# Kernel optimization log

Measured on AMD Instinct MI355X. Metric: run time of the kernel, lower is better.

## Reference

```python
import jax, jax.numpy as jnp
import numpy as np

DIM = 512
HEADS = 8
DIM_HEAD = 64
INNER = HEADS * DIM_HEAD
SCALE = DIM_HEAD ** -0.5


def setup_inputs() -> dict:
    key = jax.random.key(0)
    ks = jax.random.split(key, 7)
    B, N = 8, 1024
    x = jax.random.normal(ks[0], (B, N, DIM), dtype=jnp.float32)
    rel_pos_bias = jax.random.normal(ks[1], (HEADS, N, N), dtype=jnp.float32) * 0.02
    w_qkv = jax.random.normal(ks[2], (DIM, 3 * INNER), dtype=jnp.float32) * (DIM ** -0.5)
    w_out = jax.random.normal(ks[3], (INNER, DIM), dtype=jnp.float32) * (INNER ** -0.5)
    b_out = jnp.zeros((DIM,), dtype=jnp.float32)
    ln_gamma = jnp.ones((DIM,), dtype=jnp.float32)
    ln_beta = jnp.zeros((DIM,), dtype=jnp.float32)
    return {"x": x, "rel_pos_bias": rel_pos_bias, "w_qkv": w_qkv,
            "w_out": w_out, "b_out": b_out, "ln_gamma": ln_gamma, "ln_beta": ln_beta}


def _layernorm(x, gamma, beta, eps=1e-5):
    mu = jnp.mean(x, axis=-1, keepdims=True)
    var = jnp.var(x, axis=-1, keepdims=True)
    return (x - mu) * jax.lax.rsqrt(var + eps) * gamma + beta


def reference(x, rel_pos_bias, w_qkv, w_out, b_out, ln_gamma, ln_beta):
    B, N, _ = x.shape
    xn = _layernorm(x, ln_gamma, ln_beta)
    qkv = xn @ w_qkv  # [B,N,3*INNER]
    q, k, v = jnp.split(qkv, 3, axis=-1)
    # b n (h d) -> b h n d
    reshape = lambda t: t.reshape(B, N, HEADS, DIM_HEAD).transpose(0, 2, 1, 3)
    q, k, v = reshape(q) * SCALE, reshape(k), reshape(v)
    sim = jnp.einsum('bhid,bhjd->bhij', q, k)
    sim = sim + rel_pos_bias  # broadcast [h,N,N] over batch
    attn = jax.nn.softmax(sim, axis=-1)
    out = jnp.einsum('bhij,bhjd->bhid', attn, v)
    out = out.transpose(0, 2, 1, 3).reshape(B, N, INNER)
    return out @ w_out + b_out
```

## Files before the change

### kernel.cpp

```cpp
#include <hip/hip_runtime.h>
#include <hip/hip_bf16.h>

#define DIM 512
#define HEADS 8
#define DHEAD 64
#define INNER 512
#define NSEQ 1024
#define BATCH 8
#define MROWS (BATCH*NSEQ)
#define QK_SCALE 0.125f
#define LOG2E 1.44269504f

typedef __attribute__((ext_vector_type(4))) float f32x4;
typedef __attribute__((ext_vector_type(8))) short short8;
typedef unsigned short ushort_t;

__device__ inline ushort_t f2bf(float f) {
    __hip_bfloat16 h = __float2bfloat16(f);
    return *reinterpret_cast<ushort_t*>(&h);
}
__device__ inline float bf2f(ushort_t u) {
    union { unsigned int i; float f; } c; c.i = ((unsigned int)u) << 16; return c.f;
}
__device__ inline float fast_exp2(float x) {
    float r; asm("v_exp_f32 %0, %1" : "=v"(r) : "v"(x)); return r;
}

#define GLD16(gsrc, ldst) __builtin_amdgcn_global_load_lds( \
    (const __attribute__((address_space(1))) void*)(gsrc), \
    (__attribute__((address_space(3))) void*)(ldst), 16, 0, 0)

__device__ inline void tc_tile(const float* __restrict__ w, ushort_t* __restrict__ wt,
        int ncols, int n0, int k0, int t, ushort_t (*T)[72]) {
    int kr = t >> 2;
    int nc = (t & 3) * 16;
    const float4* src = (const float4*)(w + (size_t)(k0 + kr) * ncols + n0 + nc);
    float4 f0 = src[0], f1 = src[1], f2 = src[2], f3 = src[3];
    ushort_t tmp[16];
    tmp[0]=f2bf(f0.x); tmp[1]=f2bf(f0.y); tmp[2]=f2bf(f0.z); tmp[3]=f2bf(f0.w);
    tmp[4]=f2bf(f1.x); tmp[5]=f2bf(f1.y); tmp[6]=f2bf(f1.z); tmp[7]=f2bf(f1.w);
    tmp[8]=f2bf(f2.x); tmp[9]=f2bf(f2.y); tmp[10]=f2bf(f2.z); tmp[11]=f2bf(f2.w);
    tmp[12]=f2bf(f3.x); tmp[13]=f2bf(f3.y); tmp[14]=f2bf(f3.z); tmp[15]=f2bf(f3.w);
    *(uint4*)&T[kr][nc]     = *(uint4*)&tmp[0];
    *(uint4*)&T[kr][nc + 8] = *(uint4*)&tmp[8];
    __syncthreads();
    int nr = t >> 2;
    int kc = (t & 3) * 16;
    ushort_t o[16];
    for (int j = 0; j < 16; j++) o[j] = T[kc + j][nr];
    ushort_t* dst = wt + (size_t)(n0 + nr) * 512 + k0 + kc;
    *(uint4*)(dst)     = *(uint4*)&o[0];
    *(uint4*)(dst + 8) = *(uint4*)&o[8];
}

__global__ __launch_bounds__(256) void prep_kernel(
        const float* __restrict__ x, const float* __restrict__ gamma,
        const float* __restrict__ beta, ushort_t* __restrict__ xn,
        const float* __restrict__ w_qkv, ushort_t* __restrict__ wqkvT,
        const float* __restrict__ w_out, ushort_t* __restrict__ woutT,
        const float* __restrict__ bias, ushort_t* __restrict__ biasb) {
    __shared__ ushort_t T[64][72];
    int bid = blockIdx.x;
    int t = threadIdx.x;
    if (bid < 2048) {
        int row = bid * 4 + (t >> 6);
        int lane = t & 63;
        const float4* xr = (const float4*)(x + (size_t)row * DIM);
        float4 a0 = xr[lane];
        float4 a1 = xr[lane + 64];
        float s  = a0.x + a0.y + a0.z + a0.w + a1.x + a1.y + a1.z + a1.w;
        float ss = a0.x*a0.x + a0.y*a0.y + a0.z*a0.z + a0.w*a0.w
                 + a1.x*a1.x + a1.y*a1.y + a1.z*a1.z + a1.w*a1.w;
        for (int off = 1; off < 64; off <<= 1) {
            s  += __shfl_xor(s, off);
            ss += __shfl_xor(ss, off);
        }
        float mean = s * (1.0f / DIM);
        float var  = ss * (1.0f / DIM) - mean * mean;
        float inv  = rsqrtf(var + 1e-5f);
        const float4* g4 = (const float4*)gamma;
        const float4* b4 = (const float4*)beta;
        float4 g0 = g4[lane], g1 = g4[lane + 64];
        float4 be0 = b4[lane], be1 = b4[lane + 64];
        ushort4 o0, o1;
        o0.x = f2bf((a0.x - mean) * inv * g0.x + be0.x);
        o0.y = f2bf((a0.y - mean) * inv * g0.y + be0.y);
        o0.z = f2bf((a0.z - mean) * inv * g0.z + be0.z);
        o0.w = f2bf((a0.w - mean) * inv * g0.w + be0.w);
        o1.x = f2bf((a1.x - mean) * inv * g1.x + be1.x);
        o1.y = f2bf((a1.y - mean) * inv * g1.y + be1.y);
        o1.z = f2bf((a1.z - mean) * inv * g1.z + be1.z);
        o1.w = f2bf((a1.w - mean) * inv * g1.w + be1.w);
        ushort4* outr = (ushort4*)(xn + (size_t)row * DIM);
        outr[lane] = o0;
        outr[lane + 64] = o1;
    } else if (bid < 2240) {
        int rel = bid - 2048;
        tc_tile(w_qkv, wqkvT, 1536, (rel % 24) * 64, (rel / 24) * 64, t, T);
    } else if (bid < 2304) {
        int rel = bid - 2240;
        tc_tile(w_out, woutT, 512, (rel % 8) * 64, (rel / 8) * 64, t, T);
    } else {
        int rel = bid - 2304;
        int i = rel * 256 + t;
        float4 v = ((const float4*)bias)[i];
        ushort4 o;
        o.x = f2bf(v.x * LOG2E); o.y = f2bf(v.y * LOG2E);
        o.z = f2bf(v.z * LOG2E); o.w = f2bf(v.w * LOG2E);
        ((ushort4*)biasb)[i] = o;
    }
}

__global__ __launch_bounds__(256) void v_transpose(const ushort_t* __restrict__ vb,
        ushort_t* __restrict__ vt) {
    __shared__ ushort_t T[64][72];
    int bh = blockIdx.y;
    int s0 = blockIdx.x * 64;
    int t = threadIdx.x;
    int row = t >> 2, c = (t & 3) * 16;
    const ushort_t* src = vb + ((size_t)bh * NSEQ + s0 + row) * DHEAD + c;
    *(uint4*)&T[row][c]     = *(const uint4*)(src);
    *(uint4*)&T[row][c + 8] = *(const uint4*)(src + 8);
    __syncthreads();
    int d = t >> 2;
    int sq = (t & 3) * 16;
    ushort_t tmp[16];
    for (int j = 0; j < 16; j++) tmp[j] = T[sq + j][d];
    *(uint4*)(vt + ((size_t)bh * DHEAD + d) * NSEQ + s0 + sq)     = *(uint4*)&tmp[0];
    *(uint4*)(vt + ((size_t)bh * DHEAD + d) * NSEQ + s0 + sq + 8) = *(uint4*)&tmp[8];
}

template<int EPI, int BN>
__global__ __launch_bounds__(256) void gemm_kernel(
        const ushort_t* __restrict__ A, const ushort_t* __restrict__ Bt,
        ushort_t* __restrict__ qb, ushort_t* __restrict__ kb, ushort_t* __restrict__ vb,
        float* __restrict__ outp, const float* __restrict__ bvec) {
    constexpr int BNF = BN / 32;
    __shared__ ushort_t Als[128][32];
    __shared__ ushort_t Bls[BN][32];
    int t = threadIdx.x, lane = t & 63, w = t >> 6;
    int bm = blockIdx.y, bn = blockIdx.x;
    int wm = w >> 1, wn = w & 1;
    int l15 = lane & 15, l4 = lane >> 4;
    int lr = lane >> 2, lc = (lane & 3) * 8;

    const ushort_t* gA = A  + (size_t)(bm * 128) * DIM;
    const ushort_t* gB = Bt + (size_t)(bn * BN) * DIM;

    f32x4 acc[4][BNF] = {};

    {
        GLD16(gA + (size_t)(w*32      + lr) * DIM + lc, &Als[w*32][0]);
        GLD16(gA + (size_t)(w*32 + 16 + lr) * DIM + lc, &Als[w*32 + 16][0]);
        if constexpr (BN == 128) {
            GLD16(gB + (size_t)(w*32      + lr) * DIM + lc, &Bls[w*32][0]);
            GLD16(gB + (size_t)(w*32 + 16 + lr) * DIM + lc, &Bls[w*32 + 16][0]);
        } else {
            GLD16(gB + (size_t)(w*16 + lr) * DIM + lc, &Bls[w*16][0]);
        }
    }

    for (int kt = 0; kt < DIM / 32; ++kt) {
        __syncthreads();
        short8 af[4], bfr[BNF];
        for (int mi = 0; mi < 4; mi++)   af[mi]  = *(const short8*)&Als[wm*64 + mi*16 + l15][l4*8];
        for (int ni = 0; ni < BNF; ni++) bfr[ni] = *(const short8*)&Bls[wn*(BN/2) + ni*16 + l15][l4*8];
        __syncthreads();
        if (kt + 1 < DIM / 32) {
            int ko = (kt + 1) * 32;
            GLD16(gA + (size_t)(w*32      + lr) * DIM + ko + lc, &Als[w*32][0]);
            GLD16(gA + (size_t)(w*32 + 16 + lr) * DIM + ko + lc, &Als[w*32 + 16][0]);
            if constexpr (BN == 128) {
                GLD16(gB + (size_t)(w*32      + lr) * DIM + ko + lc, &Bls[w*32][0]);
                GLD16(gB + (size_t)(w*32 + 16 + lr) * DIM + ko + lc, &Bls[w*32 + 16][0]);
            } else {
                GLD16(gB + (size_t)(w*16 + lr) * DIM + ko + lc, &Bls[w*16][0]);
            }
        }
        for (int mi = 0; mi < 4; mi++)
            for (int ni = 0; ni < BNF; ni++)
                acc[mi][ni] = __builtin_amdgcn_mfma_f32_16x16x32_bf16(bfr[ni], af[mi], acc[mi][ni], 0, 0, 0);
    }

    for (int mi = 0; mi < 4; mi++) {
        int r = bm*128 + wm*64 + mi*16 + l15;
        for (int ni = 0; ni < BNF; ni++) {
            int c = bn*BN + wn*(BN/2) + ni*16 + l4*4;
            f32x4 v = acc[mi][ni];
            if (EPI == 0) {
                int part = c >> 9, cw = c & 511;
                int h = cw >> 6, d = cw & 63;
                int b = r >> 10, i = r & 1023;
                size_t off = (((size_t)(b*HEADS + h)) * NSEQ + i) * DHEAD + d;
                ushort4 o;
                if (part == 0) {
                    o.x = f2bf(v[0] * (QK_SCALE*LOG2E)); o.y = f2bf(v[1] * (QK_SCALE*LOG2E));
                    o.z = f2bf(v[2] * (QK_SCALE*LOG2E)); o.w = f2bf(v[3] * (QK_SCALE*LOG2E));
                    *(ushort4*)(qb + off) = o;
                } else if (part == 1) {
                    o.x = f2bf(v[0]); o.y = f2bf(v[1]); o.z = f2bf(v[2]); o.w = f2bf(v[3]);
                    *(ushort4*)(kb + off) = o;
                } else {
                    o.x = f2bf(v[0]); o.y = f2bf(v[1]); o.z = f2bf(v[2]); o.w = f2bf(v[3]);
                    *(ushort4*)(vb + off) = o;
                }
            } else {
                float4 bv = *(const float4*)(bvec + c);
                float4 o2;
                o2.x = v[0] + bv.x; o2.y = v[1] + bv.y;
                o2.z = v[2] + bv.z; o2.w = v[3] + bv.w;
                *(float4*)(outp + (size_t)r * DIM + c) = o2;
            }
        }
    }
}

__global__ __launch_bounds__(256) void attn_kernel(
        const ushort_t* __restrict__ q, const ushort_t* __restrict__ k,
        const ushort_t* __restrict__ vt, const ushort_t* __restrict__ biasb,
        ushort_t* __restrict__ attno) {
    __shared__ ushort_t Kls[64][72];
    __shared__ ushort_t Vtls[64][72];
    __shared__ ushort_t Pls[4][16][72];
    int t = threadIdx.x, lane = t & 63, w = t >> 6;
    int l15 = lane & 15, l4 = lane >> 4;
    int b = blockIdx.x, h = blockIdx.y, q0 = blockIdx.z * 64;
    size_t bh = (size_t)(b * HEADS + h);
    const ushort_t* qp = q  + (bh * NSEQ + q0 + w*16) * DHEAD;
    const ushort_t* kp = k  + bh * NSEQ * DHEAD;
    const ushort_t* vp = vt + bh * DHEAD * NSEQ;
    int qrow = q0 + w*16 + l15;
    const ushort_t* bp = biasb + ((size_t)h * NSEQ + qrow) * NSEQ;

    short8 bq[2];
    bq[0] = *(const short8*)(qp + l15*DHEAD + l4*8);
    bq[1] = *(const short8*)(qp + l15*DHEAD + l4*8 + 32);

    f32x4 o[4] = {};
    float mrun = -INFINITY, lrun = 0.f;

    int srow = t >> 2, sc = (t & 3) * 16;

    uint4 kreg0, kreg1, vreg0, vreg1;
    ushort4 cb[4], nb[4];
    {
        const ushort_t* ks0 = kp + (size_t)srow * DHEAD + sc;
        const ushort_t* vs0 = vp + (size_t)srow * NSEQ + sc;
        kreg0 = *(const uint4*)(ks0);
        kreg1 = *(const uint4*)(ks0 + 8);
        vreg0 = *(const uint4*)(vs0);
        vreg1 = *(const uint4*)(vs0 + 8);
        for (int ni = 0; ni < 4; ni++)
            cb[ni] = *(const ushort4*)(bp + ni*16 + l4*4);
    }

    for (int kt = 0; kt < NSEQ / 64; ++kt) {
        __syncthreads();
        *(uint4*)&Kls[srow][sc]      = kreg0;
        *(uint4*)&Kls[srow][sc + 8]  = kreg1;
        *(uint4*)&Vtls[srow][sc]     = vreg0;
        *(uint4*)&Vtls[srow][sc + 8] = vreg1;
        __syncthreads();

        if (kt + 1 < NSEQ / 64) {
            const ushort_t* ksn = kp + (size_t)((kt+1)*64 + srow) * DHEAD + sc;
            const ushort_t* vsn = vp + (size_t)srow * NSEQ + (kt+1)*64 + sc;
            kreg0 = *(const uint4*)(ksn);
            kreg1 = *(const uint4*)(ksn + 8);
            vreg0 = *(const uint4*)(vsn);
            vreg1 = *(const uint4*)(vsn + 8);
        }

        f32x4 s[4];
        __builtin_amdgcn_s_setprio(1);
        for (int ni = 0; ni < 4; ni++) {
            f32x4 z = {};
            short8 ak0 = *(const short8*)&Kls[ni*16 + l15][l4*8];
            short8 ak1 = *(const short8*)&Kls[ni*16 + l15][l4*8 + 32];
            z = __builtin_amdgcn_mfma_f32_16x16x32_bf16(ak0, bq[0], z, 0, 0, 0);
            z = __builtin_amdgcn_mfma_f32_16x16x32_bf16(ak1, bq[1], z, 0, 0, 0);
            s[ni] = z;
        }
        __builtin_amdgcn_s_setprio(0);

        float p[16];
        float mj = -INFINITY;
        for (int ni = 0; ni < 4; ni++) {
            ushort4 b4 = cb[ni];
            float v0 = s[ni][0] + bf2f(b4.x);
            float v1 = s[ni][1] + bf2f(b4.y);
            float v2 = s[ni][2] + bf2f(b4.z);
            float v3 = s[ni][3] + bf2f(b4.w);
            p[ni*4+0] = v0; p[ni*4+1] = v1; p[ni*4+2] = v2; p[ni*4+3] = v3;
            mj = fmaxf(mj, fmaxf(fmaxf(v0, v1), fmaxf(v2, v3)));
        }
        mj = fmaxf(mj, __shfl_xor(mj, 16));
        mj = fmaxf(mj, __shfl_xor(mj, 32));
        if (kt + 1 < NSEQ / 64) {
            for (int ni = 0; ni < 4; ni++)
                nb[ni] = *(const ushort4*)(bp + (kt+1)*64 + ni*16 + l4*4);
        }
        if (!__all(mj <= mrun + 8.f)) {
            float mnew = fmaxf(mrun, mj);
            float scl = fast_exp2(mrun - mnew);
            lrun *= scl;
            for (int di = 0; di < 4; di++) o[di] *= scl;
            mrun = mnew;
        }
        float rs = 0.f;
        for (int i = 0; i < 16; i++) {
            p[i] = fast_exp2(p[i] - mrun);
            rs += p[i];
        }
        rs += __shfl_xor(rs, 16);
        rs += __shfl_xor(rs, 32);
        lrun += rs;

        for (int ni = 0; ni < 4; ni++) {
            ushort4 pk;
            pk.x = f2bf(p[ni*4+0]); pk.y = f2bf(p[ni*4+1]);
            pk.z = f2bf(p[ni*4+2]); pk.w = f2bf(p[ni*4+3]);
            *(ushort4*)&Pls[w][l15][ni*16 + l4*4] = pk;
        }

        __builtin_amdgcn_s_setprio(1);
        for (int ks2 = 0; ks2 < 2; ks2++) {
            short8 pb = *(const short8*)&Pls[w][l15][ks2*32 + l4*8];
            for (int di = 0; di < 4; di++) {
                short8 av = *(const short8*)&Vtls[di*16 + l15][ks2*32 + l4*8];
                o[di] = __builtin_amdgcn_mfma_f32_16x16x32_bf16(av, pb, o[di], 0, 0, 0);
            }
        }
        __builtin_amdgcn_s_setprio(0);

        for (int ni = 0; ni < 4; ni++) cb[ni] = nb[ni];
    }

    float inv = 1.0f / lrun;
    for (int di = 0; di < 4; di++) {
        ushort4 ov;
        ov.x = f2bf(o[di][0] * inv);
        ov.y = f2bf(o[di][1] * inv);
        ov.z = f2bf(o[di][2] * inv);
        ov.w = f2bf(o[di][3] * inv);
        *(ushort4*)(attno + ((size_t)(b*NSEQ + qrow)) * INNER + h*DHEAD + di*16 + l4*4) = ov;
    }
}

extern "C" void kernel_launch(void* const* d_in, const int* in_sizes, int n_in,
                              void* d_out, int out_size, void* d_ws, size_t ws_size,
                              hipStream_t stream) {
    (void)in_sizes; (void)n_in; (void)out_size; (void)ws_size;
    const float* x      = (const float*)d_in[0];
    const float* bias   = (const float*)d_in[1];
    const float* w_qkv  = (const float*)d_in[2];
    const float* w_out  = (const float*)d_in[3];
    const float* b_out  = (const float*)d_in[4];
    const float* gamma  = (const float*)d_in[5];
    const float* beta   = (const float*)d_in[6];
    float* out = (float*)d_out;

    ushort_t* xn    = (ushort_t*)d_ws;
    ushort_t* wqkvT = xn + (size_t)MROWS * DIM;
    ushort_t* woutT = wqkvT + (size_t)1536 * 512;
    ushort_t* qb    = woutT + (size_t)512 * 512;
    ushort_t* kb    = qb + (size_t)MROWS * INNER;
    ushort_t* vb    = kb + (size_t)MROWS * INNER;
    ushort_t* vt    = vb + (size_t)MROWS * INNER;
    ushort_t* attn  = vt + (size_t)MROWS * INNER;
    ushort_t* biasb = attn + (size_t)MROWS * INNER;

    hipLaunchKernelGGL(prep_kernel, dim3(10496), dim3(256), 0, stream,
                       x, gamma, beta, xn, w_qkv, wqkvT, w_out, woutT, bias, biasb);
    hipLaunchKernelGGL((gemm_kernel<0, 128>), dim3(1536 / 128, MROWS / 128), dim3(256), 0, stream,
                       xn, wqkvT, qb, kb, vb, nullptr, nullptr);
    hipLaunchKernelGGL(v_transpose, dim3(NSEQ / 64, BATCH * HEADS), dim3(256), 0, stream, vb, vt);
    hipLaunchKernelGGL(attn_kernel, dim3(BATCH, HEADS, NSEQ / 64), dim3(256), 0, stream,
                       qb, kb, vt, biasb, attn);
    hipLaunchKernelGGL((gemm_kernel<1, 64>), dim3(DIM / 64, MROWS / 128), dim3(256), 0, stream,
                       attn, woutT, nullptr, nullptr, nullptr, out, b_out);
}
```

Before: 193.2 us.

## Fuse V transpose into QKV GEMM epilogue, stage epilogues in LDS, remap attention grid

The QKV GEMM now stages each wave's 64x64 output tile in shared memory and writes V directly in transposed layout, so the separate v_transpose kernel and the intermediate V buffer go away. Q/K and the output GEMM epilogues also go through LDS so that global stores are full 16-byte row-contiguous writes. The attention kernel uses a 1-D grid with an XCD-aware remap that groups blocks of the same bias head and query tile onto one XCD, aiming for better L2 reuse of the bias. The cost is extra LDS (about 36 KB per block in the QKV GEMM), which may lower occupancy.

```diff
diff --git a/kernel.cpp b/kernel.cpp
--- a/kernel.cpp
+++ b/kernel.cpp
@@ -111,33 +111,12 @@
     }
 }
 
-__global__ __launch_bounds__(256) void v_transpose(const ushort_t* __restrict__ vb,
-        ushort_t* __restrict__ vt) {
-    __shared__ ushort_t T[64][72];
-    int bh = blockIdx.y;
-    int s0 = blockIdx.x * 64;
-    int t = threadIdx.x;
-    int row = t >> 2, c = (t & 3) * 16;
-    const ushort_t* src = vb + ((size_t)bh * NSEQ + s0 + row) * DHEAD + c;
-    *(uint4*)&T[row][c]     = *(const uint4*)(src);
-    *(uint4*)&T[row][c + 8] = *(const uint4*)(src + 8);
-    __syncthreads();
-    int d = t >> 2;
-    int sq = (t & 3) * 16;
-    ushort_t tmp[16];
-    for (int j = 0; j < 16; j++) tmp[j] = T[sq + j][d];
-    *(uint4*)(vt + ((size_t)bh * DHEAD + d) * NSEQ + s0 + sq)     = *(uint4*)&tmp[0];
-    *(uint4*)(vt + ((size_t)bh * DHEAD + d) * NSEQ + s0 + sq + 8) = *(uint4*)&tmp[8];
-}
-
-template<int EPI, int BN>
-__global__ __launch_bounds__(256) void gemm_kernel(
+__global__ __launch_bounds__(256) void gemm_qkv(
         const ushort_t* __restrict__ A, const ushort_t* __restrict__ Bt,
-        ushort_t* __restrict__ qb, ushort_t* __restrict__ kb, ushort_t* __restrict__ vb,
-        float* __restrict__ outp, const float* __restrict__ bvec) {
-    constexpr int BNF = BN / 32;
+        ushort_t* __restrict__ qb, ushort_t* __restrict__ kb, ushort_t* __restrict__ vt) {
     __shared__ ushort_t Als[128][32];
-    __shared__ ushort_t Bls[BN][32];
+    __shared__ ushort_t Bls[128][32];
+    __shared__ ushort_t Tw[4][64][72];
     int t = threadIdx.x, lane = t & 63, w = t >> 6;
     int bm = blockIdx.y, bn = blockIdx.x;
     int wm = w >> 1, wn = w & 1;
@@ -145,73 +124,137 @@
     int lr = lane >> 2, lc = (lane & 3) * 8;
 
     const ushort_t* gA = A  + (size_t)(bm * 128) * DIM;
-    const ushort_t* gB = Bt + (size_t)(bn * BN) * DIM;
-
-    f32x4 acc[4][BNF] = {};
-
-    {
-        GLD16(gA + (size_t)(w*32      + lr) * DIM + lc, &Als[w*32][0]);
-        GLD16(gA + (size_t)(w*32 + 16 + lr) * DIM + lc, &Als[w*32 + 16][0]);
-        if constexpr (BN == 128) {
-            GLD16(gB + (size_t)(w*32      + lr) * DIM + lc, &Bls[w*32][0]);
-            GLD16(gB + (size_t)(w*32 + 16 + lr) * DIM + lc, &Bls[w*32 + 16][0]);
-        } else {
-            GLD16(gB + (size_t)(w*16 + lr) * DIM + lc, &Bls[w*16][0]);
-        }
-    }
+    const ushort_t* gB = Bt + (size_t)(bn * 128) * DIM;
+
+    f32x4 acc[4][4] = {};
+
+    GLD16(gA + (size_t)(w*32      + lr) * DIM + lc, &Als[w*32][0]);
+    GLD16(gA + (size_t)(w*32 + 16 + lr) * DIM + lc, &Als[w*32 + 16][0]);
+    GLD16(gB + (size_t)(w*32      + lr) * DIM + lc, &Bls[w*32][0]);
+    GLD16(gB + (size_t)(w*32 + 16 + lr) * DIM + lc, &Bls[w*32 + 16][0]);
 
     for (int kt = 0; kt < DIM / 32; ++kt) {
         __syncthreads();
-        short8 af[4], bfr[BNF];
-        for (int mi = 0; mi < 4; mi++)   af[mi]  = *(const short8*)&Als[wm*64 + mi*16 + l15][l4*8];
-        for (int ni = 0; ni < BNF; ni++) bfr[ni] = *(const short8*)&Bls[wn*(BN/2) + ni*16 + l15][l4*8];
+        short8 af[4], bfr[4];
+        for (int mi = 0; mi < 4; mi++) af[mi]  = *(const short8*)&Als[wm*64 + mi*16 + l15][l4*8];
+        for (int ni = 0; ni < 4; ni++) bfr[ni] = *(const short8*)&Bls[wn*64 + ni*16 + l15][l4*8];
         __syncthreads();
         if (kt + 1 < DIM / 32) {
             int ko = (kt + 1) * 32;
             GLD16(gA + (size_t)(w*32      + lr) * DIM + ko + lc, &Als[w*32][0]);
             GLD16(gA + (size_t)(w*32 + 16 + lr) * DIM + ko + lc, &Als[w*32 + 16][0]);
-            if constexpr (BN == 128) {
-                GLD16(gB + (size_t)(w*32      + lr) * DIM + ko + lc, &Bls[w*32][0]);
-                GLD16(gB + (size_t)(w*32 + 16 + lr) * DIM + ko + lc, &Bls[w*32 + 16][0]);
-            } else {
-                GLD16(gB + (size_t)(w*16 + lr) * DIM + ko + lc, &Bls[w*16][0]);
+            GLD16(gB + (size_t)(w*32      + lr) * DIM + ko + lc, &Bls[w*32][0]);
+            GLD16(gB + (size_t)(w*32 + 16 + lr) * DIM + ko + lc, &Bls[w*32 + 16][0]);
+        }
+        for (int mi = 0; mi < 4; mi++)
+            for (int ni = 0; ni < 4; ni++)
+                acc[mi][ni] = __builtin_amdgcn_mfma_f32_16x16x32_bf16(bfr[ni], af[mi], acc[mi][ni], 0, 0, 0);
+    }
+
+    int c0 = bn*128 + wn*64;
+    int part = c0 >> 9;
+    int h = (c0 & 511) >> 6;
+    int R0 = bm*128 + wm*64;
+    int b = R0 >> 10;
+    int i0 = R0 & 1023;
+    size_t bh = (size_t)(b * HEADS + h);
+
+    if (part == 2) {
+        for (int mi = 0; mi < 4; mi++)
+            for (int ni = 0; ni < 4; ni++) {
+                f32x4 v = acc[mi][ni];
+                for (int j = 0; j < 4; j++)
+                    Tw[w][ni*16 + l4*4 + j][mi*16 + l15] = f2bf(v[j]);
             }
-        }
+    } else {
+        float qs = (part == 0) ? (QK_SCALE * LOG2E) : 1.0f;
         for (int mi = 0; mi < 4; mi++)
-            for (int ni = 0; ni < BNF; ni++)
+            for (int ni = 0; ni < 4; ni++) {
+                f32x4 v = acc[mi][ni];
+                ushort4 o;
+                o.x = f2bf(v[0] * qs); o.y = f2bf(v[1] * qs);
+                o.z = f2bf(v[2] * qs); o.w = f2bf(v[3] * qs);
+                *(ushort4*)&Tw[w][mi*16 + l15][ni*16 + l4*4] = o;
+            }
+    }
+    __syncthreads();
+
+    int rr = lane >> 3;
+    int cc = (lane & 7) * 8;
+    if (part == 2) {
+        for (int s = 0; s < 8; s++) {
+            int dloc = s*8 + rr;
+            uint4 val = *(const uint4*)&Tw[w][dloc][cc];
+            *(uint4*)(vt + (bh * DHEAD + dloc) * NSEQ + i0 + cc) = val;
+        }
+    } else {
+        ushort_t* dst = (part == 0) ? qb : kb;
+        for (int s = 0; s < 8; s++) {
+            int iloc = s*8 + rr;
+            uint4 val = *(const uint4*)&Tw[w][iloc][cc];
+            *(uint4*)(dst + (bh * NSEQ + (i0 + iloc)) * DHEAD + cc) = val;
+        }
+    }
+}
+
+__global__ __launch_bounds__(256) void gemm_out(
+        const ushort_t* __restrict__ A, const ushort_t* __restrict__ Bt,
+        float* __restrict__ outp, const float* __restrict__ bvec) {
+    __shared__ ushort_t Als[128][32];
+    __shared__ ushort_t Bls[64][32];
+    __shared__ float Twf[4][64][36];
+    int t = threadIdx.x, lane = t & 63, w = t >> 6;
+    int bm = blockIdx.y, bn = blockIdx.x;
+    int wm = w >> 1, wn = w & 1;
+    int l15 = lane & 15, l4 = lane >> 4;
+    int lr = lane >> 2, lc = (lane & 3) * 8;
+
+    const ushort_t* gA = A  + (size_t)(bm * 128) * DIM;
+    const ushort_t* gB = Bt + (size_t)(bn * 64) * DIM;
+
+    f32x4 acc[4][2] = {};
+
+    GLD16(gA + (size_t)(w*32      + lr) * DIM + lc, &Als[w*32][0]);
+    GLD16(gA + (size_t)(w*32 + 16 + lr) * DIM + lc, &Als[w*32 + 16][0]);
+    GLD16(gB + (size_t)(w*16 + lr) * DIM + lc, &Bls[w*16][0]);
+
+    for (int kt = 0; kt < DIM / 32; ++kt) {
+        __syncthreads();
+        short8 af[4], bfr[2];
+        for (int mi = 0; mi < 4; mi++) af[mi]  = *(const short8*)&Als[wm*64 + mi*16 + l15][l4*8];
+        for (int ni = 0; ni < 2; ni++) bfr[ni] = *(const short8*)&Bls[wn*32 + ni*16 + l15][l4*8];
+        __syncthreads();
+        if (kt + 1 < DIM / 32) {
+            int ko = (kt + 1) * 32;
+            GLD16(gA + (size_t)(w*32      + lr) * DIM + ko + lc, &Als[w*32][0]);
+            GLD16(gA + (size_t)(w*32 + 16 + lr) * DIM + ko + lc, &Als[w*32 + 16][0]);
+            GLD16(gB + (size_t)(w*16 + lr) * DIM + ko + lc, &Bls[w*16][0]);
+        }
+        for (int mi = 0; mi < 4; mi++)
+            for (int ni = 0; ni < 2; ni++)
                 acc[mi][ni] = __builtin_amdgcn_mfma_f32_16x16x32_bf16(bfr[ni], af[mi], acc[mi][ni], 0, 0, 0);
     }
 
-    for (int mi = 0; mi < 4; mi++) {
-        int r = bm*128 + wm*64 + mi*16 + l15;
-        for (int ni = 0; ni < BNF; ni++) {
-            int c = bn*BN + wn*(BN/2) + ni*16 + l4*4;
+    int C0 = bn*64 + wn*32;
+    int R0 = bm*128 + wm*64;
+    for (int mi = 0; mi < 4; mi++)
+        for (int ni = 0; ni < 2; ni++) {
+            int c = C0 + ni*16 + l4*4;
+            float4 bv = *(const float4*)(bvec + c);
             f32x4 v = acc[mi][ni];
-            if (EPI == 0) {
-                int part = c >> 9, cw = c & 511;
-                int h = cw >> 6, d = cw & 63;
-                int b = r >> 10, i = r & 1023;
-                size_t off = (((size_t)(b*HEADS + h)) * NSEQ + i) * DHEAD + d;
-                ushort4 o;
-                if (part == 0) {
-                    o.x = f2bf(v[0] * (QK_SCALE*LOG2E)); o.y = f2bf(v[1] * (QK_SCALE*LOG2E));
-                    o.z = f2bf(v[2] * (QK_SCALE*LOG2E)); o.w = f2bf(v[3] * (QK_SCALE*LOG2E));
-                    *(ushort4*)(qb + off) = o;
-                } else if (part == 1) {
-                    o.x = f2bf(v[0]); o.y = f2bf(v[1]); o.z = f2bf(v[2]); o.w = f2bf(v[3]);
-                    *(ushort4*)(kb + off) = o;
-                } else {
-                    o.x = f2bf(v[0]); o.y = f2bf(v[1]); o.z = f2bf(v[2]); o.w = f2bf(v[3]);
-                    *(ushort4*)(vb + off) = o;
-                }
-            } else {
-                float4 bv = *(const float4*)(bvec + c);
-                float4 o2;
-                o2.x = v[0] + bv.x; o2.y = v[1] + bv.y;
-                o2.z = v[2] + bv.z; o2.w = v[3] + bv.w;
-                *(float4*)(outp + (size_t)r * DIM + c) = o2;
-            }
-        }
+            float4 o2;
+            o2.x = v[0] + bv.x; o2.y = v[1] + bv.y;
+            o2.z = v[2] + bv.z; o2.w = v[3] + bv.w;
+            *(float4*)&Twf[w][mi*16 + l15][ni*16 + l4*4] = o2;
+        }
+    __syncthreads();
+
+    int rr = lane >> 3;
+    int cc = (lane & 7) * 4;
+    for (int s = 0; s < 8; s++) {
+        int iloc = s*8 + rr;
+        float4 val = *(const float4*)&Twf[w][iloc][cc];
+        *(float4*)(outp + (size_t)(R0 + iloc) * DIM + C0 + cc) = val;
     }
 }
 
@@ -224,7 +267,12 @@
     __shared__ ushort_t Pls[4][16][72];
     int t = threadIdx.x, lane = t & 63, w = t >> 6;
     int l15 = lane & 15, l4 = lane >> 4;
-    int b = blockIdx.x, h = blockIdx.y, q0 = blockIdx.z * 64;
+    int bid = blockIdx.x;
+    int xcd = bid & 7, s2 = bid >> 3;
+    int g = xcd * 16 + (s2 >> 3);
+    int b = s2 & 7;
+    int h = g & 7;
+    int q0 = (g >> 3) * 64;
     size_t bh = (size_t)(b * HEADS + h);
     const ushort_t* qp = q  + (bh * NSEQ + q0 + w*16) * DHEAD;
     const ushort_t* kp = k  + bh * NSEQ * DHEAD;
@@ -365,18 +413,16 @@
     ushort_t* woutT = wqkvT + (size_t)1536 * 512;
     ushort_t* qb    = woutT + (size_t)512 * 512;
     ushort_t* kb    = qb + (size_t)MROWS * INNER;
-    ushort_t* vb    = kb + (size_t)MROWS * INNER;
-    ushort_t* vt    = vb + (size_t)MROWS * INNER;
+    ushort_t* vt    = kb + (size_t)MROWS * INNER;
     ushort_t* attn  = vt + (size_t)MROWS * INNER;
     ushort_t* biasb = attn + (size_t)MROWS * INNER;
 
     hipLaunchKernelGGL(prep_kernel, dim3(10496), dim3(256), 0, stream,
                        x, gamma, beta, xn, w_qkv, wqkvT, w_out, woutT, bias, biasb);
-    hipLaunchKernelGGL((gemm_kernel<0, 128>), dim3(1536 / 128, MROWS / 128), dim3(256), 0, stream,
-                       xn, wqkvT, qb, kb, vb, nullptr, nullptr);
-    hipLaunchKernelGGL(v_transpose, dim3(NSEQ / 64, BATCH * HEADS), dim3(256), 0, stream, vb, vt);
-    hipLaunchKernelGGL(attn_kernel, dim3(BATCH, HEADS, NSEQ / 64), dim3(256), 0, stream,
+    hipLaunchKernelGGL(gemm_qkv, dim3(1536 / 128, MROWS / 128), dim3(256), 0, stream,
+                       xn, wqkvT, qb, kb, vt);
+    hipLaunchKernelGGL(attn_kernel, dim3(BATCH * HEADS * (NSEQ / 64)), dim3(256), 0, stream,
                        qb, kb, vt, biasb, attn);
-    hipLaunchKernelGGL((gemm_kernel<1, 64>), dim3(DIM / 64, MROWS / 128), dim3(256), 0, stream,
-                       attn, woutT, nullptr, nullptr, nullptr, out, b_out);
-}
+    hipLaunchKernelGGL(gemm_out, dim3(DIM / 64, MROWS / 128), dim3(256), 0, stream,
+                       attn, woutT, out, b_out);
+}
```

Result: no change. 191.0 us (-1.1%).
